# Kernel tuning notes

Measured on AMD Instinct MI355X. Metric: run time of the kernel, lower is better.

The kernel has to match this reference:

```python
import jax, jax.numpy as jnp
import numpy as np

D = 64
H = 4
FF = 4  # fourier features
EPS = 1e-5


def _ln(x, g, b):
    m = jnp.mean(x, axis=-1, keepdims=True)
    v = jnp.mean((x - m) ** 2, axis=-1, keepdims=True)
    return (x - m) / jnp.sqrt(v + EPS) * g + b


def setup_inputs() -> dict:
    key = jax.random.key(0)
    ks = jax.random.split(key, 30)
    s = 0.05
    inp = {
        'feats': jax.random.normal(ks[0], (1, 1024, D), jnp.float32),
        'coors': jax.random.normal(ks[1], (1, 1024, 3), jnp.float32),
        'qkv_w': jax.random.normal(ks[2], (D, 3 * D), jnp.float32) * s,
        'out_w': jax.random.normal(ks[3], (D, D), jnp.float32) * s,
        'out_b': jnp.zeros((D,), jnp.float32),
        'edge_w1': jax.random.normal(ks[4], (2 * FF + 1, D), jnp.float32) * s,
        'edge_b1': jnp.zeros((D,), jnp.float32),
        'edge_w2': jax.random.normal(ks[5], (D, D), jnp.float32) * s,
        'edge_b2': jnp.zeros((D,), jnp.float32),
        'coord_w1': jax.random.normal(ks[6], (D, D), jnp.float32) * s,
        'coord_b1': jnp.zeros((D,), jnp.float32),
        'coord_w2': jax.random.normal(ks[7], (D, 1), jnp.float32) * s,
        'coord_b2': jnp.zeros((1,), jnp.float32),
        'gate_w1': jax.random.normal(ks[8], (D, D), jnp.float32) * s,
        'gate_b1': jnp.zeros((D,), jnp.float32),
        'gate_w2': jax.random.normal(ks[9], (D, 1), jnp.float32) * s,
        'gate_b2': jnp.zeros((1,), jnp.float32),
        'ln1_g': jnp.ones((D,), jnp.float32),
        'ln1_b': jnp.zeros((D,), jnp.float32),
        'ln2_g': jnp.ones((D,), jnp.float32),
        'ln2_b': jnp.zeros((D,), jnp.float32),
        'ffn_w1': jax.random.normal(ks[10], (D, 4 * D), jnp.float32) * s,
        'ffn_b1': jnp.zeros((4 * D,), jnp.float32),
        'ffn_w2': jax.random.normal(ks[11], (4 * D, D), jnp.float32) * s,
        'ffn_b2': jnp.zeros((D,), jnp.float32),
    }
    return inp


def reference(feats, coors, qkv_w, out_w, out_b, edge_w1, edge_b1, edge_w2, edge_b2,
              coord_w1, coord_b1, coord_w2, coord_b2, gate_w1, gate_b1, gate_w2, gate_b2,
              ln1_g, ln1_b, ln2_g, ln2_b, ffn_w1, ffn_b1, ffn_w2, ffn_b2):
    B, N, Dm = feats.shape
    x = _ln(feats, ln1_g, ln1_b)  # norm1 (pre-norm; also used as residual base, faithful to source)

    # pairwise relative coords and squared distance
    rel = coors[:, :, None, :] - coors[:, None, :, :]        # [B,N,N,3]
    rd = jnp.sum(rel ** 2, axis=-1, keepdims=True)            # [B,N,N,1]
    freqs = 2.0 ** jnp.arange(FF, dtype=coors.dtype)
    fr = rd / freqs                                           # [B,N,N,FF]
    enc = jnp.concatenate([jnp.sin(fr), jnp.cos(fr), rd], -1) # [B,N,N,2*FF+1]

    # edge MLP (edges=None, edge_dim=0)
    e_ij = jax.nn.silu(enc @ edge_w1 + edge_b1) @ edge_w2 + edge_b2  # [B,N,N,D]

    # attention
    qkv = x @ qkv_w
    q, k, v = jnp.split(qkv, 3, axis=-1)
    hd = Dm // H
    q = q.reshape(B, N, H, hd).transpose(0, 2, 1, 3)
    k = k.reshape(B, N, H, hd).transpose(0, 2, 1, 3)
    v = v.reshape(B, N, H, hd).transpose(0, 2, 1, 3)
    scores = jnp.einsum('bhid,bhjd->bhij', q, k) / jnp.sqrt(jnp.asarray(Dm, q.dtype))
    attn = jax.nn.softmax(scores, axis=-1)                    # [B,H,N,N]
    msg = jnp.einsum('bhij,bhjd->bhid', attn, v)
    msg = msg.transpose(0, 2, 1, 3).reshape(B, N, Dm)
    x = x + (msg @ out_w + out_b)
    x = x + (jax.nn.gelu(_ln(x, ln2_g, ln2_b) @ ffn_w1 + ffn_b1, approximate=False) @ ffn_w2 + ffn_b2)

    # coordinate update
    cw = (jax.nn.silu(e_ij @ coord_w1 + coord_b1) @ coord_w2 + coord_b2)[..., 0]  # [B,N,N]
    cw = cw * jnp.mean(attn, axis=1)
    gate = jax.nn.sigmoid(jax.nn.silu(x @ gate_w1 + gate_b1) @ gate_w2 + gate_b2)  # [B,N,1]
    delta = jnp.einsum('bij,bijd->bid', cw, rel) * gate
    return x, coors + delta
```

## Files before the change

### kernel.cpp

```cpp
#include <hip/hip_runtime.h>
#include <hip/hip_bf16.h>

#define N 1024
#define D 64

typedef __attribute__((ext_vector_type(8))) short bf16x8;
typedef __attribute__((ext_vector_type(4))) float f32x4;

__device__ __forceinline__ unsigned short f2b(float v) {
  unsigned u = __float_as_uint(v);
  u += 0x7fffu + ((u >> 16) & 1u);
  return (unsigned short)(u >> 16);
}
__device__ __forceinline__ unsigned short f2bc(float v) {
  union { __hip_bfloat16 h; unsigned short u; } r;
  r.h = __float2bfloat16(v);
  return r.u;
}
__device__ __forceinline__ unsigned pk2(float a, float b) {
  union { __hip_bfloat162 h; unsigned u; } r;
  r.h = __hip_bfloat162(__float2bfloat16(a), __float2bfloat16(b));
  return r.u;
}
__device__ __forceinline__ float bu(unsigned short u) {
  return __uint_as_float(((unsigned)u) << 16);
}
__device__ __forceinline__ float silu_f(float x) {
  return x * __builtin_amdgcn_rcpf(1.f + __expf(-x));
}
__device__ __forceinline__ float sigm_f(float x) {
  return __builtin_amdgcn_rcpf(1.f + __expf(-x));
}

__global__ __launch_bounds__(256) void k_ln1_qkv_prep(
    const float* __restrict__ feats, const float* __restrict__ g, const float* __restrict__ b,
    const float* __restrict__ qkv_w, float* __restrict__ xn, float* __restrict__ qkv,
    const float* __restrict__ ew1, const float* __restrict__ eb1,
    const float* __restrict__ ew2, const float* __restrict__ cw1,
    const float* __restrict__ eb2, const float* __restrict__ cb1,
    unsigned short* __restrict__ pw, float* __restrict__ b3p) {
  __shared__ float sh[64 * 64];
  const int t = threadIdx.x;
  if (blockIdx.x == 256) {
    float* wc = sh;
    for (int idx = t; idx < 4096; idx += 256) {
      const int r = idx >> 6, c = idx & 63;
      float s = 0.f;
#pragma unroll 8
      for (int k = 0; k < 64; ++k) s += ew2[r * 64 + k] * cw1[k * 64 + c];
      wc[idx] = s;
    }
    __syncthreads();
    for (int idx = t; idx < 12 * 512; idx += 256) {
      const int e = idx & 7, l = (idx >> 3) & 63, f = idx >> 9;
      const int l15 = l & 15, lg = l >> 4;
      float v;
      if (f < 4) {
        const int d = f * 16 + l15, k = lg * 8 + e;
        v = (k < 9) ? ew1[k * 64 + d] : (k == 9 ? eb1[d] : 0.f);
      } else {
        const int gq = f - 4, d = (gq >> 1) * 16 + l15, k = (gq & 1) * 32 + lg * 8 + e;
        v = wc[k * 64 + d];
      }
      pw[idx] = f2b(v);
    }
    if (t < 64) {
      float s = cb1[t];
#pragma unroll 8
      for (int k = 0; k < 64; ++k) s += eb2[k] * cw1[k * 64 + t];
      b3p[t] = s;
    }
    return;
  }
  const int r = t >> 6, lane = t & 63;
  const int i = blockIdx.x * 4 + r;
  float v = feats[i * D + lane];
  float s = v;
#pragma unroll
  for (int off = 32; off; off >>= 1) s += __shfl_xor(s, off);
  const float m = s * (1.0f / 64.0f);
  const float dv = v - m;
  float vs = dv * dv;
#pragma unroll
  for (int off = 32; off; off >>= 1) vs += __shfl_xor(vs, off);
  const float var = vs * (1.0f / 64.0f);
  const float xv = dv * rsqrtf(var + 1e-5f) * g[lane] + b[lane];
  xn[i * D + lane] = xv;
  float* xs = sh;
  xs[r * 64 + lane] = xv;
  __syncthreads();
#pragma unroll
  for (int c = 0; c < 3; ++c) {
    const int col = lane + c * 64;
    float acc = 0.f;
#pragma unroll 8
    for (int k = 0; k < D; ++k) acc += xs[r * 64 + k] * qkv_w[k * 192 + col];
    qkv[i * 192 + col] = acc;
  }
}

__global__ __launch_bounds__(256) void k_scores(
    const float* __restrict__ qkv, unsigned short* __restrict__ P,
    float* __restrict__ l_ws, float* __restrict__ pv_ws) {
  const int i0 = blockIdx.x * 64, j0 = blockIdx.y * 64, jb = blockIdx.y;
  const int t = threadIdx.x;
  const int lane = t & 63, h = t >> 6;
  const int l15 = lane & 15, lg = lane >> 4;
  const int r7 = l15 & 7;

  __shared__ __align__(16) unsigned short Qs[64 * 64];
  __shared__ __align__(16) unsigned short Ks[64 * 64];
  __shared__ __align__(16) unsigned short VTs[4 * 16 * 64];
  __shared__ __align__(16) unsigned short Ps[4 * 64 * 64];

  {
    const int si = t >> 2, q4 = t & 3;
    const int g0 = ((q4 * 2) ^ (si & 7)) * 8, g1 = ((q4 * 2 + 1) ^ (si & 7)) * 8;
    {
      const float* qr = &qkv[(i0 + si) * 192 + q4 * 16];
      float4 a0 = *(const float4*)(qr + 0), a1 = *(const float4*)(qr + 4);
      float4 a2 = *(const float4*)(qr + 8), a3 = *(const float4*)(qr + 12);
      *(uint4*)&Qs[si * 64 + g0] = make_uint4(
          pk2(a0.x * 0.125f, a0.y * 0.125f), pk2(a0.z * 0.125f, a0.w * 0.125f),
          pk2(a1.x * 0.125f, a1.y * 0.125f), pk2(a1.z * 0.125f, a1.w * 0.125f));
      *(uint4*)&Qs[si * 64 + g1] = make_uint4(
          pk2(a2.x * 0.125f, a2.y * 0.125f), pk2(a2.z * 0.125f, a2.w * 0.125f),
          pk2(a3.x * 0.125f, a3.y * 0.125f), pk2(a3.z * 0.125f, a3.w * 0.125f));
    }
    {
      const float* kr = &qkv[(j0 + si) * 192 + 64 + q4 * 16];
      float4 a0 = *(const float4*)(kr + 0), a1 = *(const float4*)(kr + 4);
      float4 a2 = *(const float4*)(kr + 8), a3 = *(const float4*)(kr + 12);
      *(uint4*)&Ks[si * 64 + g0] = make_uint4(pk2(a0.x, a0.y), pk2(a0.z, a0.w),
                                              pk2(a1.x, a1.y), pk2(a1.z, a1.w));
      *(uint4*)&Ks[si * 64 + g1] = make_uint4(pk2(a2.x, a2.y), pk2(a2.z, a2.w),
                                              pk2(a3.x, a3.y), pk2(a3.z, a3.w));
    }
    {
      const float* vr = &qkv[(j0 + si) * 192 + 128 + q4 * 16];
      float4 v0 = *(const float4*)(vr + 0), v1 = *(const float4*)(vr + 4);
      float4 v2 = *(const float4*)(vr + 8), v3 = *(const float4*)(vr + 12);
      float vv[16] = {v0.x, v0.y, v0.z, v0.w, v1.x, v1.y, v1.z, v1.w,
                      v2.x, v2.y, v2.z, v2.w, v3.x, v3.y, v3.z, v3.w};
      const int sj3 = si >> 3, sj7 = si & 7;
#pragma unroll
      for (int cc = 0; cc < 16; ++cc)
        VTs[q4 * 1024 + cc * 64 + ((sj3 ^ (cc & 7)) * 8) + sj7] = f2bc(vv[cc]);
    }
  }
  __syncthreads();

  const bf16x8 z8 = {0, 0, 0, 0, 0, 0, 0, 0};
  const int gk = ((h * 2 + (lg & 1)) ^ r7) * 8;
  bf16x8 qa[4], kb[4];
#pragma unroll
  for (int it = 0; it < 4; ++it) {
    qa[it] = *(const bf16x8*)&Qs[(it * 16 + l15) * 64 + gk];
    if (lg >= 2) qa[it] = z8;
    kb[it] = *(const bf16x8*)&Ks[(it * 16 + l15) * 64 + gk];
  }
  f32x4 acc[4][4];
#pragma unroll
  for (int it = 0; it < 4; ++it)
#pragma unroll
    for (int jt = 0; jt < 4; ++jt)
      acc[it][jt] = (f32x4){0.f, 0.f, 0.f, 0.f};
#pragma unroll
  for (int it = 0; it < 4; ++it)
#pragma unroll
    for (int jt = 0; jt < 4; ++jt)
      acc[it][jt] = __builtin_amdgcn_mfma_f32_16x16x32_bf16(qa[it], kb[jt], acc[it][jt], 0, 0, 0);

  float prow[4][4];
#pragma unroll
  for (int it = 0; it < 4; ++it)
#pragma unroll
    for (int rr = 0; rr < 4; ++rr) prow[it][rr] = 0.f;
#pragma unroll
  for (int it = 0; it < 4; ++it)
#pragma unroll
    for (int jt = 0; jt < 4; ++jt)
#pragma unroll
      for (int rr = 0; rr < 4; ++rr) {
        const float p = __expf(acc[it][jt][rr]);
        prow[it][rr] += p;
        const int irow = it * 16 + lg * 4 + rr;
        const int col = jt * 16 + l15;
        Ps[h * 4096 + irow * 64 + (((col >> 3) ^ (irow & 7)) * 8) + (col & 7)] = f2bc(p);
      }
#pragma unroll
  for (int it = 0; it < 4; ++it)
#pragma unroll
    for (int rr = 0; rr < 4; ++rr) {
      float s = prow[it][rr];
      s += __shfl_xor(s, 1); s += __shfl_xor(s, 2);
      s += __shfl_xor(s, 4); s += __shfl_xor(s, 8);
      if (l15 == 0)
        l_ws[h * 16384 + jb * 1024 + i0 + it * 16 + lg * 4 + rr] = s;
    }

  f32x4 av[4];
#pragma unroll
  for (int it = 0; it < 4; ++it) av[it] = (f32x4){0.f, 0.f, 0.f, 0.f};
#pragma unroll
  for (int ks = 0; ks < 2; ++ks) {
    const int gj = ((ks * 4 + lg) ^ r7) * 8;
    bf16x8 vb = *(const bf16x8*)&VTs[h * 1024 + l15 * 64 + gj];
#pragma unroll
    for (int it = 0; it < 4; ++it) {
      bf16x8 pa = *(const bf16x8*)&Ps[h * 4096 + (it * 16 + l15) * 64 + gj];
      av[it] = __builtin_amdgcn_mfma_f32_16x16x32_bf16(pa, vb, av[it], 0, 0, 0);
    }
  }
#pragma unroll
  for (int it = 0; it < 4; ++it)
#pragma unroll
    for (int rr = 0; rr < 4; ++rr)
      pv_ws[jb * 65536 + (i0 + it * 16 + lg * 4 + rr) * 64 + h * 16 + l15] = av[it][rr];

  {
    const int ir = t & 63;
    unsigned short* pg = &P[h * 1048576 + (i0 + ir) * 1024 + j0];
#pragma unroll
    for (int gg = 0; gg < 8; ++gg)
      *(uint4*)&pg[gg * 8] = *(const uint4*)&Ps[h * 4096 + ir * 64 + ((gg ^ (ir & 7)) * 8)];
  }
}

__global__ __launch_bounds__(256) void k_meanattn(
    const unsigned short* P, const float* __restrict__ l_ws, unsigned short* ma) {
  const int i0 = blockIdx.x * 64, j0 = blockIdx.y * 64;
  const int t = threadIdx.x;
  __shared__ float invl[4][64];
  {
    const int h = t >> 6, r = t & 63;
    float s = 0.f;
#pragma unroll
    for (int jt = 0; jt < 16; ++jt) s += l_ws[h * 16384 + jt * 1024 + i0 + r];
    invl[h][r] = 0.25f * __builtin_amdgcn_rcpf(s);
  }
  __syncthreads();
  {
    const int r = t >> 2, cg = t & 3;
    float v[16];
#pragma unroll
    for (int k = 0; k < 16; ++k) v[k] = 0.f;
#pragma unroll
    for (int h = 0; h < 4; ++h) {
      const unsigned short* pr = &P[h * 1048576 + (i0 + r) * 1024 + j0 + cg * 16];
      uint4 a = *(const uint4*)pr;
      uint4 b2 = *(const uint4*)(pr + 8);
      const float sh = invl[h][r];
      unsigned uu[8] = {a.x, a.y, a.z, a.w, b2.x, b2.y, b2.z, b2.w};
#pragma unroll
      for (int q = 0; q < 8; ++q) {
        v[q * 2 + 0] += sh * bu((unsigned short)(uu[q] & 0xffffu));
        v[q * 2 + 1] += sh * bu((unsigned short)(uu[q] >> 16));
      }
    }
    unsigned out[8];
#pragma unroll
    for (int q = 0; q < 8; ++q) out[q] = pk2(v[2 * q], v[2 * q + 1]);
    unsigned short* mr = &ma[(i0 + r) * 1024 + j0 + cg * 16];
    *(uint4*)mr = make_uint4(out[0], out[1], out[2], out[3]);
    *(uint4*)(mr + 8) = make_uint4(out[4], out[5], out[6], out[7]);
  }
}

__global__ __launch_bounds__(256) void k_ffn_gate(
    const float* __restrict__ pv_ws, const float* __restrict__ l_ws,
    const float* __restrict__ xn,
    const float* __restrict__ out_w, const float* __restrict__ out_b,
    const float* __restrict__ ln2_g, const float* __restrict__ ln2_b,
    const float* __restrict__ fw1, const float* __restrict__ fb1,
    const float* __restrict__ fw2, const float* __restrict__ fb2,
    const float* __restrict__ gw1, const float* __restrict__ gb1,
    const float* __restrict__ gw2, const float* __restrict__ gb2,
    float* __restrict__ xout, float* __restrict__ gate) {
  const int i = blockIdx.x, t = threadIdx.x;
  __shared__ float msgv[64], xs[64], x1s[64], hs[256];
  if (t < 64) {
    float ls = 0.f;
#pragma unroll
    for (int jt = 0; jt < 16; ++jt) ls += l_ws[(t >> 4) * 16384 + jt * 1024 + i];
    const float invh = __builtin_amdgcn_rcpf(ls);
    float s = 0.f;
#pragma unroll
    for (int jt = 0; jt < 16; ++jt) s += pv_ws[jt * 65536 + i * 64 + t];
    msgv[t] = s * invh;
  }
  __syncthreads();
  if (t < 64) {
    float o = out_b[t];
#pragma unroll 8
    for (int k = 0; k < 64; ++k) o += msgv[k] * out_w[k * 64 + t];
    const float v = xn[i * 64 + t] + o;
    x1s[t] = v;
    float s = v;
#pragma unroll
    for (int off = 32; off; off >>= 1) s += __shfl_xor(s, off);
    const float m = s * (1.f / 64.f);
    const float dv = v - m;
    float vs = dv * dv;
#pragma unroll
    for (int off = 32; off; off >>= 1) vs += __shfl_xor(vs, off);
    xs[t] = dv * rsqrtf(vs * (1.f / 64.f) + 1e-5f) * ln2_g[t] + ln2_b[t];
  }
  __syncthreads();
  float a = fb1[t];
#pragma unroll 8
  for (int k = 0; k < 64; ++k) a += xs[k] * fw1[k * 256 + t];
  const float ge = 0.5f * a * (1.f + erff(a * 0.70710678118f));
  hs[t] = ge;
  __syncthreads();
  if (t < 64) {
    float o = fb2[t];
#pragma unroll 8
    for (int k = 0; k < 256; ++k) o += hs[k] * fw2[k * 64 + t];
    const float xo = x1s[t] + o;
    xout[i * 64 + t] = xo;
    xs[t] = xo;
  }
  __syncthreads();
  if (t < 64) {
    float a2 = gb1[t];
#pragma unroll 8
    for (int k = 0; k < 64; ++k) a2 += xs[k] * gw1[k * 64 + t];
    const float sg = a2 * sigm_f(a2);
    float pp = sg * gw2[t];
#pragma unroll
    for (int off = 32; off; off >>= 1) pp += __shfl_xor(pp, off);
    if (t == 0) gate[i] = sigm_f(pp + gb2[0]);
  }
}

__global__ __launch_bounds__(256) void k_pair(
    const float* __restrict__ coors, const unsigned short* __restrict__ ma,
    const unsigned short* __restrict__ pw,
    const float* __restrict__ b3p, const float* __restrict__ c2g,
    const float* __restrict__ cb2, float* __restrict__ partial) {
  const int b = blockIdx.x;
  int ti, tj, h;
  bool diag;
  if (b < 992) {
    const int q = b >> 1;
    h = b & 1;
    int bb = q;
    ti = 0;
    while (bb >= 31 - ti) { bb -= 31 - ti; ++ti; }
    tj = ti + 1 + bb;
    diag = false;
  } else {
    ti = tj = b - 992;
    h = 0;
    diag = true;
  }

  const int t = threadIdx.x;
  const int w = t >> 6;
  const int lane = t & 63;
  const int l15 = lane & 15;
  const int lg = lane >> 4;

  __shared__ __align__(16) unsigned short buf[4][2][32][64];
  __shared__ float4 relA[4][2][32], relB[4][2][32];
  __shared__ float di[4][32][3], dj[4][32][3];

  bf16x8 wf[12];
#pragma unroll
  for (int f = 0; f < 12; ++f)
    wf[f] = *(const bf16x8*)&pw[(f * 64 + lane) * 8];

  float b3v[16], c2v[16];
#pragma unroll
  for (int mt = 0; mt < 4; ++mt)
#pragma unroll
    for (int r = 0; r < 4; ++r) {
      const int d = mt * 16 + lg * 4 + r;
      b3v[mt * 4 + r] = b3p[d];
      c2v[mt * 4 + r] = c2g[d];
    }
  const float cb2q = cb2[0];
  if (lane < 32) {
    const int j = lane;
#pragma unroll
    for (int k2 = 0; k2 < 3; ++k2) { di[w][j][k2] = 0.f; dj[w][j][k2] = 0.f; }
    const uint4 z4 = make_uint4(0, 0, 0, 0);
#pragma unroll
    for (int s = 0; s < 2; ++s) {
      unsigned short* rp = &buf[w][s][j][0];
      *(uint4*)&rp[(1 ^ (j & 7)) * 8] = z4;
      *(uint4*)&rp[(2 ^ (j & 7)) * 8] = z4;
      *(uint4*)&rp[(3 ^ (j & 7)) * 8] = z4;
    }
  }

  f32x4 acc[2][4][2];

  for (int u = 0; u < 2; ++u) {
    int dgnb[2];
#pragma unroll
    for (int s = 0; s < 2; ++s) {
      const int c = u * 2 + s;
      dgnb[s] = diag ? (c * 4 + w + 1) : (h * 16 + c * 4 + w);
    }

#pragma unroll
    for (int s = 0; s < 2; ++s) {
      const int dgn = dgnb[s];
      const int p = lane & 31;
      const int hhalf = lane >> 5;
      const int ig = ti * 32 + p;
      const int jj = (p + dgn) & 31;
      const int jg = tj * 32 + jj;
      const float rx = coors[ig * 3 + 0] - coors[jg * 3 + 0];
      const float ry = coors[ig * 3 + 1] - coors[jg * 3 + 1];
      const float rz = coors[ig * 3 + 2] - coors[jg * 3 + 2];
      const float rd = rx * rx + ry * ry + rz * rz;
      unsigned short* rp = &buf[w][s][p][0];
      if (hhalf == 0) {
        float mi = bu(ma[ig * 1024 + jg]);
        float mj = bu(ma[jg * 1024 + ig]);
        if (diag && dgn == 16 && p >= 16) { mi = 0.f; mj = 0.f; }
        relA[w][s][p] = make_float4(mi * rx, mi * ry, mi * rz, 0.f);
        relB[w][s][p] = make_float4(mj * rx, mj * ry, mj * rz, 0.f);
        *(uint2*)&rp[(0 ^ (p & 7)) * 8] =
            make_uint2(pk2(__sinf(rd), __sinf(rd * 0.5f)),
                       pk2(__sinf(rd * 0.25f), __sinf(rd * 0.125f)));
        *(unsigned*)&rp[(1 ^ (p & 7)) * 8] = pk2(rd, 1.0f);
      } else {
        *(uint2*)&rp[((0 ^ (p & 7)) * 8) + 4] =
            make_uint2(pk2(__cosf(rd), __cosf(rd * 0.5f)),
                       pk2(__cosf(rd * 0.25f), __cosf(rd * 0.125f)));
      }
    }

#pragma unroll
    for (int s = 0; s < 2; ++s)
#pragma unroll
      for (int mt = 0; mt < 4; ++mt)
#pragma unroll
        for (int nt = 0; nt < 2; ++nt)
          acc[s][mt][nt] = (f32x4){0.f, 0.f, 0.f, 0.f};
    {
      bf16x8 bf0[2], bf1[2];
      const int j0 = l15, j1 = 16 + l15;
#pragma unroll
      for (int s = 0; s < 2; ++s) {
        bf0[s] = *(const bf16x8*)&buf[w][s][j0][(lg ^ (j0 & 7)) * 8];
        bf1[s] = *(const bf16x8*)&buf[w][s][j1][(lg ^ (j1 & 7)) * 8];
      }
#pragma unroll
      for (int mt = 0; mt < 4; ++mt)
#pragma unroll
        for (int s = 0; s < 2; ++s) {
          acc[s][mt][0] = __builtin_amdgcn_mfma_f32_16x16x32_bf16(wf[mt], bf0[s], acc[s][mt][0], 0, 0, 0);
          acc[s][mt][1] = __builtin_amdgcn_mfma_f32_16x16x32_bf16(wf[mt], bf1[s], acc[s][mt][1], 0, 0, 0);
        }
    }

#pragma unroll
    for (int s = 0; s < 2; ++s)
#pragma unroll
      for (int mt = 0; mt < 4; ++mt)
#pragma unroll
        for (int nt = 0; nt < 2; ++nt) {
          const f32x4 a = acc[s][mt][nt];
          const unsigned lo = pk2(silu_f(a[0]), silu_f(a[1]));
          const unsigned hi = pk2(silu_f(a[2]), silu_f(a[3]));
          const int j = nt * 16 + l15;
          const int g = mt * 2 + (lg >> 1);
          *(uint2*)&buf[w][s][j][((g ^ (j & 7)) * 8) + (lg & 1) * 4] = make_uint2(lo, hi);
        }

#pragma unroll
    for (int s = 0; s < 2; ++s)
#pragma unroll
      for (int mt = 0; mt < 4; ++mt)
#pragma unroll
        for (int nt = 0; nt < 2; ++nt)
          acc[s][mt][nt] = (f32x4){b3v[mt * 4 + 0], b3v[mt * 4 + 1], b3v[mt * 4 + 2], b3v[mt * 4 + 3]};
#pragma unroll
    for (int ks = 0; ks < 2; ++ks) {
      const int gi = ks * 4 + lg;
      const int j0 = l15, j1 = 16 + l15;
      bf16x8 bf0[2], bf1[2];
#pragma unroll
      for (int s = 0; s < 2; ++s) {
        bf0[s] = *(const bf16x8*)&buf[w][s][j0][(gi ^ (j0 & 7)) * 8];
        bf1[s] = *(const bf16x8*)&buf[w][s][j1][(gi ^ (j1 & 7)) * 8];
      }
#pragma unroll
      for (int mt = 0; mt < 4; ++mt)
#pragma unroll
        for (int s = 0; s < 2; ++s) {
          acc[s][mt][0] = __builtin_amdgcn_mfma_f32_16x16x32_bf16(wf[4 + mt * 2 + ks], bf0[s], acc[s][mt][0], 0, 0, 0);
          acc[s][mt][1] = __builtin_amdgcn_mfma_f32_16x16x32_bf16(wf[4 + mt * 2 + ks], bf1[s], acc[s][mt][1], 0, 0, 0);
        }
    }

#pragma unroll
    for (int s = 0; s < 2; ++s) {
      const int dgn = dgnb[s];
#pragma unroll
      for (int nt = 0; nt < 2; ++nt) {
        float cwp = cb2q;
#pragma unroll
        for (int mt = 0; mt < 4; ++mt) {
          const f32x4 a = acc[s][mt][nt];
#pragma unroll
          for (int r = 0; r < 4; ++r) cwp += silu_f(a[r]) * c2v[mt * 4 + r];
        }
        cwp += __shfl_xor(cwp, 16);
        cwp += __shfl_xor(cwp, 32);
        if (lg == 0) {
          const int p = nt * 16 + l15;
          const int jj = (p + dgn) & 31;
          const float4 rA = relA[w][s][p];
          const float4 rB = relB[w][s][p];
          di[w][p][0] += cwp * rA.x; di[w][p][1] += cwp * rA.y; di[w][p][2] += cwp * rA.z;
          dj[w][jj][0] -= cwp * rB.x; dj[w][jj][1] -= cwp * rB.y; dj[w][jj][2] -= cwp * rB.z;
        }
      }
    }
  }

  __syncthreads();
  if (!diag) {
    if (t < 96) {
      const int p = t / 3, k = t % 3;
      const float s = di[0][p][k] + di[1][p][k] + di[2][p][k] + di[3][p][k];
      partial[(tj * 2 + h) * 3072 + (ti * 32 + p) * 3 + k] = s;
    } else if (t < 192) {
      const int u = t - 96, q2 = u / 3, k = u % 3;
      const float s = dj[0][q2][k] + dj[1][q2][k] + dj[2][q2][k] + dj[3][q2][k];
      partial[(ti * 2 + h) * 3072 + (tj * 32 + q2) * 3 + k] = s;
    }
  } else {
    if (t < 96) {
      const int p = t / 3, k = t % 3;
      const float s = di[0][p][k] + di[1][p][k] + di[2][p][k] + di[3][p][k]
                    + dj[0][p][k] + dj[1][p][k] + dj[2][p][k] + dj[3][p][k];
      partial[(ti * 2) * 3072 + (ti * 32 + p) * 3 + k] = s;
    }
  }
}

__global__ __launch_bounds__(256) void k_finalize(
    const float* __restrict__ coors, const float* __restrict__ partial,
    const float* __restrict__ gate, float* __restrict__ outc) {
  const int idx = blockIdx.x * 256 + threadIdx.x;
  if (idx < 3072) {
    float s = 0.f;
#pragma unroll
    for (int sl = 0; sl < 64; ++sl) s += partial[sl * 3072 + idx];
    outc[idx] = coors[idx] + s * gate[idx / 3];
  }
}

extern "C" void kernel_launch(void* const* d_in, const int* in_sizes, int n_in,
                              void* d_out, int out_size, void* d_ws, size_t ws_size,
                              hipStream_t stream) {
  const float* feats = (const float*)d_in[0];
  const float* coors = (const float*)d_in[1];
  const float* qkv_w = (const float*)d_in[2];
  const float* out_w = (const float*)d_in[3];
  const float* out_b = (const float*)d_in[4];
  const float* ew1 = (const float*)d_in[5];
  const float* eb1 = (const float*)d_in[6];
  const float* ew2 = (const float*)d_in[7];
  const float* eb2 = (const float*)d_in[8];
  const float* cw1 = (const float*)d_in[9];
  const float* cb1 = (const float*)d_in[10];
  const float* cw2 = (const float*)d_in[11];
  const float* cb2 = (const float*)d_in[12];
  const float* gw1 = (const float*)d_in[13];
  const float* gb1 = (const float*)d_in[14];
  const float* gw2 = (const float*)d_in[15];
  const float* gb2 = (const float*)d_in[16];
  const float* ln1_g = (const float*)d_in[17];
  const float* ln1_b = (const float*)d_in[18];
  const float* ln2_g = (const float*)d_in[19];
  const float* ln2_b = (const float*)d_in[20];
  const float* fw1 = (const float*)d_in[21];
  const float* fb1 = (const float*)d_in[22];
  const float* fw2 = (const float*)d_in[23];
  const float* fb2 = (const float*)d_in[24];

  float* ws = (float*)d_ws;
  float* xn = ws;
  float* qkv = ws + 65536;
  float* gate = ws + 262144;
  unsigned short* pw = (unsigned short*)(ws + 263168);
  float* b3p = ws + 266240;
  float* l_ws = ws + 266304;
  float* pv_ws = ws + 331840;
  float* partial = ws + 1380416;
  unsigned short* P = (unsigned short*)(ws + 1577024);
  unsigned short* ma = P;

  float* xout = (float*)d_out;
  float* coorout = xout + 65536;

  hipLaunchKernelGGL(k_ln1_qkv_prep, dim3(257), dim3(256), 0, stream,
                     feats, ln1_g, ln1_b, qkv_w, xn, qkv,
                     ew1, eb1, ew2, cw1, eb2, cb1, pw, b3p);
  hipLaunchKernelGGL(k_scores, dim3(16, 16), dim3(256), 0, stream, qkv, P, l_ws, pv_ws);
  hipLaunchKernelGGL(k_meanattn, dim3(16, 16), dim3(256), 0, stream, P, l_ws, ma);
  hipLaunchKernelGGL(k_ffn_gate, dim3(N), dim3(256), 0, stream, pv_ws, l_ws, xn,
                     out_w, out_b, ln2_g, ln2_b,
                     fw1, fb1, fw2, fb2, gw1, gb1, gw2, gb2, xout, gate);
  hipLaunchKernelGGL(k_pair, dim3(1024), dim3(256), 0, stream, coors, ma, pw,
                     b3p, cw2, cb2, partial);
  hipLaunchKernelGGL(k_finalize, dim3(12), dim3(256), 0, stream, coors, partial, gate, coorout);
}
```

Baseline: 105.0 us.

## Merge meanattn and FFN kernels and parallelize weight prep across blocks

Combines the independent mean-attention and FFN/gate kernels into a single launch using block-index dispatch, removing a launch and the serialization between them. The fused edge/coord weight precompute, previously done by a single block, is spread across 16 extra blocks with each thread computing one packed entry directly. This shortens the tail of the front kernel at the cost of redundant global reads of the weights.

New measurement: 89.62 us. 1.17x faster.

```diff
diff --git a/kernel.cpp b/kernel.cpp
--- a/kernel.cpp
+++ b/kernel.cpp
@@ -32,46 +32,41 @@
   return __builtin_amdgcn_rcpf(1.f + __expf(-x));
 }
 
-__global__ __launch_bounds__(256) void k_ln1_qkv_prep(
+__global__ __launch_bounds__(256) void k_front(
     const float* __restrict__ feats, const float* __restrict__ g, const float* __restrict__ b,
     const float* __restrict__ qkv_w, float* __restrict__ xn, float* __restrict__ qkv,
     const float* __restrict__ ew1, const float* __restrict__ eb1,
     const float* __restrict__ ew2, const float* __restrict__ cw1,
     const float* __restrict__ eb2, const float* __restrict__ cb1,
     unsigned short* __restrict__ pw, float* __restrict__ b3p) {
-  __shared__ float sh[64 * 64];
   const int t = threadIdx.x;
-  if (blockIdx.x == 256) {
-    float* wc = sh;
-    for (int idx = t; idx < 4096; idx += 256) {
-      const int r = idx >> 6, c = idx & 63;
+  if (blockIdx.x >= 256) {
+    const int pt = (blockIdx.x - 256) * 256 + t;
+    if (pt < 2048) {
+      const int f = pt >> 9, rem = pt & 511, e = rem & 7, l = (rem >> 3) & 63;
+      const int l15 = l & 15, lg = l >> 4;
+      const int d = f * 16 + l15, k = lg * 8 + e;
+      const float v = (k < 9) ? ew1[k * 64 + d] : (k == 9 ? eb1[d] : 0.f);
+      pw[pt] = f2b(v);
+    }
+    {
+      const int f = 4 + (pt >> 9), rem = pt & 511, e = rem & 7, l = (rem >> 3) & 63;
+      const int l15 = l & 15, lg = l >> 4;
+      const int gq = f - 4, d = (gq >> 1) * 16 + l15, k = (gq & 1) * 32 + lg * 8 + e;
       float s = 0.f;
 #pragma unroll 8
-      for (int k = 0; k < 64; ++k) s += ew2[r * 64 + k] * cw1[k * 64 + c];
-      wc[idx] = s;
-    }
-    __syncthreads();
-    for (int idx = t; idx < 12 * 512; idx += 256) {
-      const int e = idx & 7, l = (idx >> 3) & 63, f = idx >> 9;
-      const int l15 = l & 15, lg = l >> 4;
-      float v;
-      if (f < 4) {
-        const int d = f * 16 + l15, k = lg * 8 + e;
-        v = (k < 9) ? ew1[k * 64 + d] : (k == 9 ? eb1[d] : 0.f);
-      } else {
-        const int gq = f - 4, d = (gq >> 1) * 16 + l15, k = (gq & 1) * 32 + lg * 8 + e;
-        v = wc[k * 64 + d];
-      }
-      pw[idx] = f2b(v);
-    }
-    if (t < 64) {
-      float s = cb1[t];
+      for (int m = 0; m < 64; ++m) s += ew2[k * 64 + m] * cw1[m * 64 + d];
+      pw[f * 512 + rem] = f2b(s);
+    }
+    if (pt < 64) {
+      float s = cb1[pt];
 #pragma unroll 8
-      for (int k = 0; k < 64; ++k) s += eb2[k] * cw1[k * 64 + t];
-      b3p[t] = s;
+      for (int k = 0; k < 64; ++k) s += eb2[k] * cw1[k * 64 + pt];
+      b3p[pt] = s;
     }
     return;
   }
+  __shared__ float xs[4 * 64];
   const int r = t >> 6, lane = t & 63;
   const int i = blockIdx.x * 4 + r;
   float v = feats[i * D + lane];
@@ -86,7 +81,6 @@
   const float var = vs * (1.0f / 64.0f);
   const float xv = dv * rsqrtf(var + 1e-5f) * g[lane] + b[lane];
   xn[i * D + lane] = xv;
-  float* xs = sh;
   xs[r * 64 + lane] = xv;
   __syncthreads();
 #pragma unroll
@@ -227,49 +221,9 @@
   }
 }
 
-__global__ __launch_bounds__(256) void k_meanattn(
-    const unsigned short* P, const float* __restrict__ l_ws, unsigned short* ma) {
-  const int i0 = blockIdx.x * 64, j0 = blockIdx.y * 64;
-  const int t = threadIdx.x;
-  __shared__ float invl[4][64];
-  {
-    const int h = t >> 6, r = t & 63;
-    float s = 0.f;
-#pragma unroll
-    for (int jt = 0; jt < 16; ++jt) s += l_ws[h * 16384 + jt * 1024 + i0 + r];
-    invl[h][r] = 0.25f * __builtin_amdgcn_rcpf(s);
-  }
-  __syncthreads();
-  {
-    const int r = t >> 2, cg = t & 3;
-    float v[16];
-#pragma unroll
-    for (int k = 0; k < 16; ++k) v[k] = 0.f;
-#pragma unroll
-    for (int h = 0; h < 4; ++h) {
-      const unsigned short* pr = &P[h * 1048576 + (i0 + r) * 1024 + j0 + cg * 16];
-      uint4 a = *(const uint4*)pr;
-      uint4 b2 = *(const uint4*)(pr + 8);
-      const float sh = invl[h][r];
-      unsigned uu[8] = {a.x, a.y, a.z, a.w, b2.x, b2.y, b2.z, b2.w};
-#pragma unroll
-      for (int q = 0; q < 8; ++q) {
-        v[q * 2 + 0] += sh * bu((unsigned short)(uu[q] & 0xffffu));
-        v[q * 2 + 1] += sh * bu((unsigned short)(uu[q] >> 16));
-      }
-    }
-    unsigned out[8];
-#pragma unroll
-    for (int q = 0; q < 8; ++q) out[q] = pk2(v[2 * q], v[2 * q + 1]);
-    unsigned short* mr = &ma[(i0 + r) * 1024 + j0 + cg * 16];
-    *(uint4*)mr = make_uint4(out[0], out[1], out[2], out[3]);
-    *(uint4*)(mr + 8) = make_uint4(out[4], out[5], out[6], out[7]);
-  }
-}
-
-__global__ __launch_bounds__(256) void k_ffn_gate(
-    const float* __restrict__ pv_ws, const float* __restrict__ l_ws,
-    const float* __restrict__ xn,
+__global__ __launch_bounds__(256) void k_mid(
+    const unsigned short* P, const float* __restrict__ l_ws, unsigned short* ma,
+    const float* __restrict__ pv_ws, const float* __restrict__ xn,
     const float* __restrict__ out_w, const float* __restrict__ out_b,
     const float* __restrict__ ln2_g, const float* __restrict__ ln2_b,
     const float* __restrict__ fw1, const float* __restrict__ fb1,
@@ -277,8 +231,51 @@
     const float* __restrict__ gw1, const float* __restrict__ gb1,
     const float* __restrict__ gw2, const float* __restrict__ gb2,
     float* __restrict__ xout, float* __restrict__ gate) {
-  const int i = blockIdx.x, t = threadIdx.x;
-  __shared__ float msgv[64], xs[64], x1s[64], hs[256];
+  __shared__ float smem[448];
+  const int t = threadIdx.x;
+  if (blockIdx.x < 256) {
+    const int i0 = (blockIdx.x >> 4) * 64, j0 = (blockIdx.x & 15) * 64;
+    float* invl = smem;
+    {
+      const int h = t >> 6, r = t & 63;
+      float s = 0.f;
+#pragma unroll
+      for (int jt = 0; jt < 16; ++jt) s += l_ws[h * 16384 + jt * 1024 + i0 + r];
+      invl[h * 64 + r] = 0.25f * __builtin_amdgcn_rcpf(s);
+    }
+    __syncthreads();
+    {
+      const int r = t >> 2, cg = t & 3;
+      float v[16];
+#pragma unroll
+      for (int k = 0; k < 16; ++k) v[k] = 0.f;
+#pragma unroll
+      for (int h = 0; h < 4; ++h) {
+        const unsigned short* pr = &P[h * 1048576 + (i0 + r) * 1024 + j0 + cg * 16];
+        uint4 a = *(const uint4*)pr;
+        uint4 b2 = *(const uint4*)(pr + 8);
+        const float sh = invl[h * 64 + r];
+        unsigned uu[8] = {a.x, a.y, a.z, a.w, b2.x, b2.y, b2.z, b2.w};
+#pragma unroll
+        for (int q = 0; q < 8; ++q) {
+          v[q * 2 + 0] += sh * bu((unsigned short)(uu[q] & 0xffffu));
+          v[q * 2 + 1] += sh * bu((unsigned short)(uu[q] >> 16));
+        }
+      }
+      unsigned out[8];
+#pragma unroll
+      for (int q = 0; q < 8; ++q) out[q] = pk2(v[2 * q], v[2 * q + 1]);
+      unsigned short* mr = &ma[(i0 + r) * 1024 + j0 + cg * 16];
+      *(uint4*)mr = make_uint4(out[0], out[1], out[2], out[3]);
+      *(uint4*)(mr + 8) = make_uint4(out[4], out[5], out[6], out[7]);
+    }
+    return;
+  }
+  const int i = blockIdx.x - 256;
+  float* msgv = smem;
+  float* xs = smem + 64;
+  float* x1s = smem + 128;
+  float* hs = smem + 192;
   if (t < 64) {
     float ls = 0.f;
 #pragma unroll
@@ -602,13 +599,12 @@
   float* xout = (float*)d_out;
   float* coorout = xout + 65536;
 
-  hipLaunchKernelGGL(k_ln1_qkv_prep, dim3(257), dim3(256), 0, stream,
+  hipLaunchKernelGGL(k_front, dim3(272), dim3(256), 0, stream,
                      feats, ln1_g, ln1_b, qkv_w, xn, qkv,
                      ew1, eb1, ew2, cw1, eb2, cb1, pw, b3p);
   hipLaunchKernelGGL(k_scores, dim3(16, 16), dim3(256), 0, stream, qkv, P, l_ws, pv_ws);
-  hipLaunchKernelGGL(k_meanattn, dim3(16, 16), dim3(256), 0, stream, P, l_ws, ma);
-  hipLaunchKernelGGL(k_ffn_gate, dim3(N), dim3(256), 0, stream, pv_ws, l_ws, xn,
-                     out_w, out_b, ln2_g, ln2_b,
+  hipLaunchKernelGGL(k_mid, dim3(1280), dim3(256), 0, stream, P, l_ws, ma,
+                     pv_ws, xn, out_w, out_b, ln2_g, ln2_b,
                      fw1, fb1, fw2, fb2, gw1, gb1, gw2, gb2, xout, gate);
   hipLaunchKernelGGL(k_pair, dim3(1024), dim3(256), 0, stream, coors, ma, pw,
                      b3p, cw2, cb2, partial);
```
